# Optimization experiments

Measured on AMD Instinct MI355X. Metric: run time of the kernel, lower is better.

## Reference

```python
import jax, jax.numpy as jnp
import numpy as np

B, NE, NR, A = 512, 100000, 400, 256
ENT, REL, HIST = 200, 200, 400
ADIM = ENT + REL  # 400
HUGE = 1e31
EPS = 1e-20


def _linear(x, W, b):
    return x @ W.T + b


def setup_inputs() -> dict:
    key = jax.random.key(0)
    ks = jax.random.split(key, 26)
    w = lambda k, o, i: (jax.random.normal(k, (o, i)) * 0.02).astype(jnp.float32)
    bz = lambda o: jnp.zeros((o,), jnp.float32)
    inp = {}
    inp['H'] = jax.random.normal(ks[0], (B, HIST), jnp.float32)
    mask = (jax.random.uniform(ks[1], (B, A)) > 0.3).astype(jnp.float32)
    inp['action_mask'] = mask.at[:, 0].set(1.0)  # ensure at least one valid action
    inp['entity_emb'] = jax.random.normal(ks[2], (NE, ENT), jnp.float32) * 0.1
    inp['relation_emb'] = jax.random.normal(ks[3], (NR, REL), jnp.float32) * 0.1
    inp['W1'] = w(ks[4], ADIM, ENT + HIST + REL); inp['b1'] = bz(ADIM)
    inp['W2'] = w(ks[5], ADIM, ADIM); inp['b2'] = bz(ADIM)
    inp['W3'] = w(ks[6], REL, ENT); inp['b3'] = bz(REL)
    inp['W4'] = w(ks[7], REL, REL); inp['b4'] = bz(REL)
    inp['W5'] = w(ks[8], REL, REL + ENT); inp['b5'] = bz(REL)
    inp['W6'] = w(ks[9], REL, REL + REL); inp['b6'] = bz(REL)
    inp['Watt'] = w(ks[10], REL, ADIM + REL); inp['batt'] = bz(REL)
    inp['e'] = jax.random.randint(ks[11], (B,), 0, NE)
    inp['q'] = jax.random.randint(ks[12], (B,), 0, NR)
    inp['pred_id'] = jax.random.randint(ks[13], (B, 1), 0, NE)
    inp['r_space'] = jax.random.randint(ks[14], (B, A), 0, NR)
    inp['e_space'] = jax.random.randint(ks[15], (B, A), 0, NE)
    return inp


def reference(H, action_mask, entity_emb, relation_emb,
              W1, b1, W2, b2, W3, b3, W4, b4, W5, b5, W6, b6, Watt, batt,
              e, q, pred_id, r_space, e_space):
    # --- embed lookups ---
    Q = relation_emb[q]                 # [B, REL]
    E = entity_emb[e]                   # [B, ENT]
    # --- small MLP (dropout in eval mode -> identity) ---
    X = jax.nn.relu(_linear(jnp.concatenate([E, H, Q], -1), W1, b1))
    X2 = _linear(X, W2, b2)             # [B, ADIM]
    # --- full relation attention (multinomial sample replaced by given pred_id) ---
    pred_emb = entity_emb[pred_id]      # [B, 1, ENT]
    pred_ent_info = _linear(pred_emb, W3, b3)       # [B, 1, REL]
    relation_K = _linear(relation_emb, W4, b4)      # [NR, REL]
    local_att = jnp.einsum('bkd,rd->bkr', pred_ent_info, relation_K)  # [B,1,NR]
    beta = jnp.einsum('bkr,rd->bkd', jax.nn.softmax(local_att, -1), relation_emb).sum(1)  # [B, REL]
    # cat([R_all expand, pred_emb expand], -1).sum(1) == [sum_r R_all, NR * pred_emb]
    rel_sum = relation_emb.sum(0)                   # [REL]
    alpha_in = jnp.concatenate([jnp.broadcast_to(rel_sum, (H.shape[0], REL)),
                                NR * pred_emb[:, 0, :]], -1)
    alpha = _linear(alpha_in, W5, b5)               # [B, REL]
    V_A = _linear(jnp.concatenate([alpha, beta], -1), W6, b6)  # [B, REL]
    relation_att = jax.nn.softmax(
        _linear(jnp.concatenate([X2, V_A], -1), Watt, batt) @ relation_emb.T, -1)  # [B, NR]
    # --- policy_nn_fun: action embedding gather + masked softmax ---
    A_emb = jnp.concatenate([relation_emb[r_space], entity_emb[e_space]], -1)  # [B, A, ADIM]
    scores = jnp.einsum('bad,bd->ba', A_emb, X2) - (1.0 - action_mask) * HUGE
    action_dist = jax.nn.softmax(scores, -1)        # [B, A]
    entropy = -jnp.sum(action_dist * jnp.log(action_dist + EPS), -1)  # [B]
    return action_dist, entropy, relation_att
```

## Files before the change

### kernel.cpp

```cpp
#include <hip/hip_runtime.h>
#include <cstdint>
#include <cstddef>

#define BB 512
#define NEn 100000
#define NRr 400
#define AA 256
#define ENTd 200
#define RELd 200
#define HISTd 400
#define ADIMd 400

__device__ __forceinline__ float dot4(const float4 a, const float4 b) {
  return a.x * b.x + a.y * b.y + a.z * b.z + a.w * b.w;
}
__device__ __forceinline__ void fma4(float4& a, const float4 w, const float c) {
  a.x += w.x * c; a.y += w.y * c; a.z += w.z * c; a.w += w.w * c;
}
__device__ __forceinline__ float wave_rmax(float v) {
#pragma unroll
  for (int off = 32; off > 0; off >>= 1) v = fmaxf(v, __shfl_xor(v, off));
  return v;
}
__device__ __forceinline__ float wave_rsum(float v) {
#pragma unroll
  for (int off = 32; off > 0; off >>= 1) v += __shfl_xor(v, off);
  return v;
}

__global__ __launch_bounds__(256) void prep1_kernel(
    const float* __restrict__ rel_emb, const float* __restrict__ W4,
    const float* __restrict__ b4, const float* __restrict__ W5,
    const float* __restrict__ b5, const float* __restrict__ W6,
    const float* __restrict__ Watt, const float* __restrict__ W1,
    const float* __restrict__ W2, float* __restrict__ RK,
    float* __restrict__ P, float* __restrict__ W6bb, float* __restrict__ ab,
    float* __restrict__ relT, float* __restrict__ WaT,
    float* __restrict__ W1T, float* __restrict__ W2T) {
  int t = threadIdx.x;
  int blk = blockIdx.x;
  if (blk == 0) {
    __shared__ float rs[RELd];
    if (t < RELd) {
      float s = 0.f;
      for (int r = 0; r < NRr; r += 4) {
        s += rel_emb[(size_t)r * RELd + t] + rel_emb[(size_t)(r + 1) * RELd + t] +
             rel_emb[(size_t)(r + 2) * RELd + t] + rel_emb[(size_t)(r + 3) * RELd + t];
      }
      rs[t] = s;
    }
    __syncthreads();
    if (t < RELd) {
      float acc = b5[t];
      const float4* w = (const float4*)(W5 + (size_t)t * 400);
      const float4* rv = (const float4*)rs;
      for (int k = 0; k < 50; ++k) acc += dot4(w[k], rv[k]);
      ab[t] = acc;
    }
  } else if (blk <= 50) {
    int r0 = (blk - 1) * 8;
    __shared__ float re[8][RELd];
    for (int i = t; i < 8 * RELd; i += 256)
      re[i / RELd][i % RELd] = rel_emb[(size_t)(r0 + i / RELd) * RELd + i % RELd];
    __syncthreads();
    if (t < RELd) {
      float bv = b4[t];
      float acc[8];
#pragma unroll
      for (int s = 0; s < 8; ++s) acc[s] = bv;
      const float4* w = (const float4*)(W4 + (size_t)t * RELd);
      for (int k = 0; k < 50; ++k) {
        float4 wv = w[k];
#pragma unroll
        for (int s = 0; s < 8; ++s) acc[s] += dot4(wv, ((const float4*)re[s])[k]);
      }
#pragma unroll
      for (int s = 0; s < 8; ++s) RK[(size_t)(r0 + s) * RELd + t] = acc[s];
    }
  } else if (blk <= 75) {
    int i0 = (blk - 51) * 8;
    __shared__ float w6s[8][200];
    for (int i = t; i < 8 * 200; i += 256)
      w6s[i / 200][i % 200] = W6[(size_t)(i0 + i / 200) * 400 + i % 200];
    __syncthreads();
    if (t < 200) {
      int k = t;
      float acc[8] = {0, 0, 0, 0, 0, 0, 0, 0};
      for (int j = 0; j < 200; j += 4) {
        float r0v = W5[(size_t)j * 400 + 200 + k];
        float r1v = W5[(size_t)(j + 1) * 400 + 200 + k];
        float r2v = W5[(size_t)(j + 2) * 400 + 200 + k];
        float r3v = W5[(size_t)(j + 3) * 400 + 200 + k];
#pragma unroll
        for (int s = 0; s < 8; ++s)
          acc[s] += w6s[s][j] * r0v + w6s[s][j + 1] * r1v + w6s[s][j + 2] * r2v +
                    w6s[s][j + 3] * r3v;
      }
#pragma unroll
      for (int s = 0; s < 8; ++s) P[(size_t)(i0 + s) * 200 + k] = 400.f * acc[s];
    }
  } else if (blk <= 100) {
    int u0 = (blk - 76) * 8;
    __shared__ float wbs[8][200];
    for (int i = t; i < 8 * 200; i += 256)
      wbs[i / 200][i % 200] = Watt[(size_t)(u0 + i / 200) * 600 + 400 + i % 200];
    __syncthreads();
    if (t < 200) {
      int j = t;
      float acc[8] = {0, 0, 0, 0, 0, 0, 0, 0};
      for (int i = 0; i < 200; i += 4) {
        float r0v = W6[(size_t)i * 400 + 200 + j];
        float r1v = W6[(size_t)(i + 1) * 400 + 200 + j];
        float r2v = W6[(size_t)(i + 2) * 400 + 200 + j];
        float r3v = W6[(size_t)(i + 3) * 400 + 200 + j];
#pragma unroll
        for (int s = 0; s < 8; ++s)
          acc[s] += wbs[s][i] * r0v + wbs[s][i + 1] * r1v + wbs[s][i + 2] * r2v +
                    wbs[s][i + 3] * r3v;
      }
#pragma unroll
      for (int s = 0; s < 8; ++s) W6bb[(size_t)(u0 + s) * 200 + j] = acc[s];
    }
  } else {
    __shared__ float tlds[64][65];
    int tb = blk - 101;
    const float* src;
    float* dst;
    int M, N, LD, ti, tj;
    if (tb < 28) {
      src = rel_emb; dst = relT; M = 400; N = 200; LD = 200;
      ti = tb / 4; tj = tb % 4;
    } else if (tb < 56) {
      tb -= 28;
      src = Watt; dst = WaT; M = 200; N = 400; LD = 600;
      ti = tb / 7; tj = tb % 7;
    } else if (tb < 147) {
      tb -= 56;
      src = W1; dst = W1T; M = 400; N = 800; LD = 800;
      ti = tb / 13; tj = tb % 13;
    } else {
      tb -= 147;
      src = W2; dst = W2T; M = 400; N = 400; LD = 400;
      ti = tb / 7; tj = tb % 7;
    }
    int i0 = ti * 64, j0 = tj * 64;
    for (int idx = t; idx < 4096; idx += 256) {
      int r = idx >> 6, c = idx & 63;
      int i = i0 + r, j = j0 + c;
      if (i < M && j < N) tlds[r][c] = src[(size_t)i * LD + j];
    }
    __syncthreads();
    for (int idx = t; idx < 4096; idx += 256) {
      int r = idx >> 6, c = idx & 63;
      int j = j0 + r, i = i0 + c;
      if (i < M && j < N) dst[(size_t)j * M + i] = tlds[c][r];
    }
  }
}

__global__ __launch_bounds__(1024) void prep2_x1_kernel(
    const float* __restrict__ rel_emb, const float* __restrict__ W3,
    const float* __restrict__ b3, const float* __restrict__ W6,
    const float* __restrict__ Watt, const float* __restrict__ batt,
    const float* __restrict__ b6, const float* __restrict__ RK,
    const float* __restrict__ P, const float* __restrict__ W6bb,
    const float* __restrict__ ab, float* __restrict__ S_T,
    float* __restrict__ cvec, float* __restrict__ Q_T,
    float* __restrict__ REatt, float* __restrict__ v1,
    const float* __restrict__ ent_emb, const float* __restrict__ H,
    const int* __restrict__ e_idx, const int* __restrict__ q_idx,
    const float* __restrict__ W1T, const float* __restrict__ b1,
    float* __restrict__ X) {
  int t = threadIdx.x;
  int blk = blockIdx.x;
  if (blk < 50) {
    int r0 = blk * 8;
    __shared__ float rks[8][200];
    __shared__ float b3s[200];
    for (int i = t; i < 1600; i += 1024)
      rks[i / 200][i % 200] = RK[(size_t)r0 * 200 + i];
    if (t < 200) b3s[t] = b3[t];
    __syncthreads();
    if (t < 200) {
      int i = t;
      float acc[8] = {0, 0, 0, 0, 0, 0, 0, 0};
      for (int j = 0; j < 200; j += 4) {
        float w0 = W3[(size_t)j * 200 + i];
        float w1 = W3[(size_t)(j + 1) * 200 + i];
        float w2 = W3[(size_t)(j + 2) * 200 + i];
        float w3v = W3[(size_t)(j + 3) * 200 + i];
#pragma unroll
        for (int s = 0; s < 8; ++s)
          acc[s] += w0 * rks[s][j] + w1 * rks[s][j + 1] + w2 * rks[s][j + 2] +
                    w3v * rks[s][j + 3];
      }
      float4 s0 = make_float4(acc[0], acc[1], acc[2], acc[3]);
      float4 s1 = make_float4(acc[4], acc[5], acc[6], acc[7]);
      *(float4*)(S_T + (size_t)i * 400 + r0) = s0;
      *(float4*)(S_T + (size_t)i * 400 + r0 + 4) = s1;
    }
    if (t < 256) {
      int w = t >> 6, lane = t & 63;
      float p0 = 0.f, p1 = 0.f;
      for (int j = lane; j < 200; j += 64) {
        p0 += b3s[j] * rks[w][j];
        p1 += b3s[j] * rks[w + 4][j];
      }
      p0 = wave_rsum(p0);
      p1 = wave_rsum(p1);
      if (lane == 0) {
        cvec[r0 + w] = p0;
        cvec[r0 + w + 4] = p1;
      }
    }
  } else if (blk < 75) {
    int u0 = (blk - 50) * 8;
    __shared__ float wbs[8][200];
    for (int i = t; i < 1600; i += 1024)
      wbs[i / 200][i % 200] = Watt[(size_t)(u0 + i / 200) * 600 + 400 + i % 200];
    __syncthreads();
    if (t < 200) {
      int k = t;
      float acc[8] = {0, 0, 0, 0, 0, 0, 0, 0};
      for (int i = 0; i < 200; i += 4) {
        float r0v = P[(size_t)i * 200 + k];
        float r1v = P[(size_t)(i + 1) * 200 + k];
        float r2v = P[(size_t)(i + 2) * 200 + k];
        float r3v = P[(size_t)(i + 3) * 200 + k];
#pragma unroll
        for (int s = 0; s < 8; ++s)
          acc[s] += wbs[s][i] * r0v + wbs[s][i + 1] * r1v + wbs[s][i + 2] * r2v +
                    wbs[s][i + 3] * r3v;
      }
      float4 s0 = make_float4(acc[0], acc[1], acc[2], acc[3]);
      float4 s1 = make_float4(acc[4], acc[5], acc[6], acc[7]);
      *(float4*)(Q_T + (size_t)k * 200 + u0) = s0;
      *(float4*)(Q_T + (size_t)k * 200 + u0 + 4) = s1;
    }
  } else if (blk < 125) {
    int r0 = (blk - 75) * 8;
    __shared__ float rels[8][200];
    for (int i = t; i < 1600; i += 1024)
      rels[i / 200][i % 200] = rel_emb[(size_t)r0 * 200 + i];
    __syncthreads();
    if (t < 200) {
      float acc[8] = {0, 0, 0, 0, 0, 0, 0, 0};
      const float4* w = (const float4*)(W6bb + (size_t)t * 200);
      for (int k = 0; k < 50; ++k) {
        float4 wv = w[k];
#pragma unroll
        for (int s = 0; s < 8; ++s) acc[s] += dot4(wv, ((const float4*)rels[s])[k]);
      }
#pragma unroll
      for (int s = 0; s < 8; ++s) REatt[(size_t)(r0 + s) * 200 + t] = acc[s];
    }
  } else if (blk == 125) {
    __shared__ float abs_[200];
    __shared__ float us[200];
    if (t < 200) abs_[t] = ab[t];
    __syncthreads();
    if (t < 200) {
      float u = b6[t];
      const float4* w = (const float4*)(W6 + (size_t)t * 400);
      const float4* rv = (const float4*)abs_;
      for (int k = 0; k < 50; ++k) u += dot4(w[k], rv[k]);
      us[t] = u;
    }
    __syncthreads();
    if (t < 200) {
      float v = batt[t];
      const float4* w = (const float4*)(Watt + (size_t)t * 600 + 400);
      const float4* rv = (const float4*)us;
      for (int k = 0; k < 50; ++k) v += dot4(w[k], rv[k]);
      v1[t] = v;
    }
  } else {
    int b0 = (blk - 126) * 4;
    __shared__ float cv[4][800];
    __shared__ float prt[12800];
    for (int i = t; i < 3200; i += 1024) {
      int s = i / 800, k = i % 800;
      float v;
      if (k < ENTd)
        v = ent_emb[(size_t)e_idx[b0 + s] * ENTd + k];
      else if (k < ENTd + HISTd)
        v = H[(size_t)(b0 + s) * HISTd + (k - ENTd)];
      else
        v = rel_emb[(size_t)q_idx[b0 + s] * RELd + (k - ENTd - HISTd)];
      cv[s][k] = v;
    }
    __syncthreads();
    if (t < 800) {
      int g = t % 100, h = t / 100;
      float4 acc[4];
#pragma unroll
      for (int s = 0; s < 4; ++s) acc[s] = make_float4(0, 0, 0, 0);
      const float4* wp = ((const float4*)W1T) + g;
      int k0 = h * 100;
#pragma unroll 4
      for (int kk = 0; kk < 100; ++kk) {
        int k = k0 + kk;
        float4 wv = wp[(size_t)k * 100];
#pragma unroll
        for (int s = 0; s < 4; ++s) fma4(acc[s], wv, cv[s][k]);
      }
#pragma unroll
      for (int s = 0; s < 4; ++s)
        ((float4*)prt)[(h * 4 + s) * 100 + g] = acc[s];
    }
    __syncthreads();
    for (int i = t; i < 1600; i += 1024) {
      int s = i / 400, j = i % 400;
      float a = b1[j];
#pragma unroll
      for (int h = 0; h < 8; ++h) a += prt[(h * 4 + s) * 400 + j];
      X[(size_t)(b0 + s) * ADIMd + j] = fmaxf(a, 0.f);
    }
  }
}

__global__ __launch_bounds__(1024) void x2rx_scores_kernel(
    const float* __restrict__ X, const float* __restrict__ W2T,
    const float* __restrict__ b2, const float* __restrict__ relT,
    const float* __restrict__ ent_emb, const int* __restrict__ r_space,
    const int* __restrict__ e_space, const float* __restrict__ mask,
    float* __restrict__ X2, float* __restrict__ out_dist,
    float* __restrict__ out_ent) {
  int b0 = blockIdx.x * 2;
  int t = threadIdx.x;
  int w = t >> 6, lane = t & 63;
  __shared__ float cv[2][400];
  __shared__ float prt[6400];
  __shared__ float x2full[2][400];
  __shared__ float rxl[2][400];
  __shared__ float scl[512];
  __shared__ float wred2[2][4];
  for (int i = t; i < 800; i += 1024) cv[i / 400][i % 400] = X[(size_t)b0 * 400 + i];
  __syncthreads();
  if (t < 800) {
    int g = t % 100, h = t / 100;
    float4 accA = make_float4(0, 0, 0, 0);
    float4 accB = make_float4(0, 0, 0, 0);
    const float4* wp = ((const float4*)W2T) + g;
    int k0 = h * 50;
#pragma unroll 4
    for (int kk = 0; kk < 50; ++kk) {
      int k = k0 + kk;
      float4 wv = wp[(size_t)k * 100];
      fma4(accA, wv, cv[0][k]);
      fma4(accB, wv, cv[1][k]);
    }
    ((float4*)prt)[(h * 2 + 0) * 100 + g] = accA;
    ((float4*)prt)[(h * 2 + 1) * 100 + g] = accB;
  }
  __syncthreads();
  if (t < 800) {
    int s = t / 400, j = t % 400;
    float a = b2[j];
#pragma unroll
    for (int h = 0; h < 8; ++h) a += prt[(h * 2 + s) * 400 + j];
    X2[(size_t)(b0 + s) * ADIMd + j] = a;
    x2full[s][j] = a;
  }
  __syncthreads();
  if (t < 800) {
    int g = t % 100, h = t / 100;
    float4 accA = make_float4(0, 0, 0, 0);
    float4 accB = make_float4(0, 0, 0, 0);
    const float4* rp = ((const float4*)relT) + g;
    int k0 = h * 25;
#pragma unroll 5
    for (int kk = 0; kk < 25; ++kk) {
      int k = k0 + kk;
      float4 wv = rp[(size_t)k * 100];
      fma4(accA, wv, x2full[0][k]);
      fma4(accB, wv, x2full[1][k]);
    }
    ((float4*)prt)[(h * 2 + 0) * 100 + g] = accA;
    ((float4*)prt)[(h * 2 + 1) * 100 + g] = accB;
  }
  __syncthreads();
  if (t < 800) {
    int s = t / 400, r = t % 400;
    float a = 0.f;
#pragma unroll
    for (int h = 0; h < 8; ++h) a += prt[(h * 2 + s) * 400 + r];
    rxl[s][r] = a;
  }
  __syncthreads();
  {
    int s = w >> 3;
    int wa = (w & 7) * 32;
    const float4* xh = ((const float4*)x2full[s]) + 50;
    for (int c = 0; c < 2; ++c) {
      int abase = wa + c * 16;
      int ei[16];
#pragma unroll
      for (int u = 0; u < 16; ++u)
        ei[u] = e_space[(size_t)(b0 + s) * AA + abase + u];
      float p[16];
      if (lane < 50) {
        float4 xv = xh[lane];
#pragma unroll
        for (int u = 0; u < 16; ++u) {
          float4 vv = ((const float4*)(ent_emb + (size_t)ei[u] * ENTd))[lane];
          p[u] = dot4(vv, xv);
        }
      } else {
#pragma unroll
        for (int u = 0; u < 16; ++u) p[u] = 0.f;
      }
#pragma unroll
      for (int off = 32; off > 0; off >>= 1) {
#pragma unroll
        for (int u = 0; u < 16; ++u) p[u] += __shfl_xor(p[u], off);
      }
      if (lane == 0) {
#pragma unroll
        for (int u = 0; u < 16; ++u) scl[s * 256 + abase + u] = p[u];
      }
    }
  }
  __syncthreads();
  float sc = -INFINITY;
  if (t < 512) {
    int s = t / 256, a = t % 256;
    int r = r_space[(size_t)(b0 + s) * AA + a];
    sc = scl[t] + rxl[s][r] - (1.f - mask[(size_t)(b0 + s) * AA + a]) * 1e31f;
  }
  if (w < 8) {
    float m = wave_rmax(sc);
    if (lane == 0) wred2[w >> 2][w & 3] = m;
  }
  __syncthreads();
  float e = 0.f;
  if (t < 512) {
    int s = t / 256;
    float gm = fmaxf(fmaxf(wred2[s][0], wred2[s][1]),
                     fmaxf(wred2[s][2], wred2[s][3]));
    e = expf(sc - gm);
  }
  __syncthreads();
  if (w < 8) {
    float s2 = wave_rsum(e);
    if (lane == 0) wred2[w >> 2][w & 3] = s2;
  }
  __syncthreads();
  float p = 0.f;
  if (t < 512) {
    int s = t / 256;
    float gs = wred2[s][0] + wred2[s][1] + wred2[s][2] + wred2[s][3];
    p = e / gs;
    out_dist[(size_t)(b0 + s) * AA + (t % 256)] = p;
  }
  float ent = (t < 512) ? -p * logf(p + 1e-20f) : 0.f;
  __syncthreads();
  if (w < 8) {
    float s3 = wave_rsum(ent);
    if (lane == 0) wred2[w >> 2][w & 3] = s3;
  }
  __syncthreads();
  if (t == 0)
    out_ent[b0] = wred2[0][0] + wred2[0][1] + wred2[0][2] + wred2[0][3];
  if (t == 1)
    out_ent[b0 + 1] = wred2[1][0] + wred2[1][1] + wred2[1][2] + wred2[1][3];
}

__global__ __launch_bounds__(1024) void fused_mid_kernel(
    const float* __restrict__ ent_emb, const int* __restrict__ pred_id,
    const float* __restrict__ X2, const float* __restrict__ S_T,
    const float* __restrict__ cvec, const float* __restrict__ Q_T,
    const float* __restrict__ REatt, const float* __restrict__ relT,
    const float* __restrict__ WaT, const float* __restrict__ v1c,
    float* __restrict__ out_ratt) {
  int t = threadIdx.x;
  int w = t >> 6, lane = t & 63;
  __shared__ float pes[4][200];
  __shared__ float x2s[4][400];
  __shared__ float pp[4][400];
  __shared__ float av[4][200];
  __shared__ float prt[12800];
  __shared__ float wred[4][4];
  int b0 = blockIdx.x * 4;
  for (int i = t; i < 2400; i += 1024) {
    if (i < 800)
      pes[i / 200][i % 200] =
          ent_emb[(size_t)pred_id[b0 + i / 200] * ENTd + i % 200];
    else {
      int k = i - 800;
      x2s[k / 400][k % 400] = X2[(size_t)b0 * 400 + k];
    }
  }
  __syncthreads();
  if (t < 800) {
    int g = t % 100, h = t / 100;
    float4 acc[4];
#pragma unroll
    for (int s = 0; s < 4; ++s) acc[s] = make_float4(0, 0, 0, 0);
    const float4* sp = ((const float4*)S_T) + g;
    int k0 = h * 25;
#pragma unroll 5
    for (int kk = 0; kk < 25; ++kk) {
      int k = k0 + kk;
      float4 wv = sp[(size_t)k * 100];
#pragma unroll
      for (int s = 0; s < 4; ++s) fma4(acc[s], wv, pes[s][k]);
    }
#pragma unroll
    for (int s = 0; s < 4; ++s)
      ((float4*)prt)[(h * 4 + s) * 100 + g] = acc[s];
  }
  __syncthreads();
  for (int i = t; i < 1600; i += 1024) {
    int s = i / 400, r = i % 400;
    float a = cvec[r];
#pragma unroll
    for (int h = 0; h < 8; ++h) a += prt[(h * 4 + s) * 400 + r];
    pp[s][r] = a;
  }
  __syncthreads();
  int row = w >> 2, q = w & 3;
  {
    float m = -INFINITY;
    for (int r = q * 64 + lane; r < 400; r += 256) m = fmaxf(m, pp[row][r]);
    m = wave_rmax(m);
    if (lane == 0) wred[row][q] = m;
    __syncthreads();
    float gm = fmaxf(fmaxf(wred[row][0], wred[row][1]),
                     fmaxf(wred[row][2], wred[row][3]));
    __syncthreads();
    float sum = 0.f;
    for (int r = q * 64 + lane; r < 400; r += 256) {
      float e = expf(pp[row][r] - gm);
      pp[row][r] = e;
      sum += e;
    }
    sum = wave_rsum(sum);
    if (lane == 0) wred[row][q] = sum;
    __syncthreads();
    float inv =
        1.f / (wred[row][0] + wred[row][1] + wred[row][2] + wred[row][3]);
    for (int r = q * 64 + lane; r < 400; r += 256) pp[row][r] *= inv;
  }
  __syncthreads();
  if (t < 800) {
    int g = t % 50, h = t / 50;
    float4 acc[4];
    if (h == 0) {
      float4 v = ((const float4*)v1c)[g];
#pragma unroll
      for (int s = 0; s < 4; ++s) acc[s] = v;
    } else {
#pragma unroll
      for (int s = 0; s < 4; ++s) acc[s] = make_float4(0, 0, 0, 0);
    }
    {
      const float4* wp = ((const float4*)WaT) + g;
      int k0 = h * 25;
#pragma unroll 5
      for (int kk = 0; kk < 25; ++kk) {
        int k = k0 + kk;
        float4 wv = wp[(size_t)k * 50];
#pragma unroll
        for (int s = 0; s < 4; ++s) fma4(acc[s], wv, x2s[s][k]);
      }
    }
    if (h < 8) {
      const float4* qp = ((const float4*)Q_T) + g;
      int k0 = h * 25;
#pragma unroll 5
      for (int kk = 0; kk < 25; ++kk) {
        int k = k0 + kk;
        float4 wv = qp[(size_t)k * 50];
#pragma unroll
        for (int s = 0; s < 4; ++s) fma4(acc[s], wv, pes[s][k]);
      }
    }
    {
      const float4* rp = ((const float4*)REatt) + g;
      int r0 = h * 25;
#pragma unroll 5
      for (int kk = 0; kk < 25; ++kk) {
        int r = r0 + kk;
        float4 wv = rp[(size_t)r * 50];
#pragma unroll
        for (int s = 0; s < 4; ++s) fma4(acc[s], wv, pp[s][r]);
      }
    }
#pragma unroll
    for (int s = 0; s < 4; ++s)
      ((float4*)prt)[(h * 4 + s) * 50 + g] = acc[s];
  }
  __syncthreads();
  if (t < 800) {
    int s = t / 200, j = t % 200;
    float a = 0.f;
#pragma unroll
    for (int h = 0; h < 16; ++h) a += prt[(h * 4 + s) * 200 + j];
    av[s][j] = a;
  }
  __syncthreads();
  if (t < 800) {
    int g = t % 100, h = t / 100;
    float4 acc[4];
#pragma unroll
    for (int s = 0; s < 4; ++s) acc[s] = make_float4(0, 0, 0, 0);
    const float4* rp = ((const float4*)relT) + g;
    int k0 = h * 25;
#pragma unroll 5
    for (int kk = 0; kk < 25; ++kk) {
      int k = k0 + kk;
      float4 wv = rp[(size_t)k * 100];
#pragma unroll
      for (int s = 0; s < 4; ++s) fma4(acc[s], wv, av[s][k]);
    }
#pragma unroll
    for (int s = 0; s < 4; ++s)
      ((float4*)prt)[(h * 4 + s) * 100 + g] = acc[s];
  }
  __syncthreads();
  for (int i = t; i < 1600; i += 1024) {
    int s = i / 400, r = i % 400;
    float a = 0.f;
#pragma unroll
    for (int h = 0; h < 8; ++h) a += prt[(h * 4 + s) * 400 + r];
    pp[s][r] = a;
  }
  __syncthreads();
  {
    float m = -INFINITY;
    for (int r = q * 64 + lane; r < 400; r += 256) m = fmaxf(m, pp[row][r]);
    m = wave_rmax(m);
    if (lane == 0) wred[row][q] = m;
    __syncthreads();
    float gm = fmaxf(fmaxf(wred[row][0], wred[row][1]),
                     fmaxf(wred[row][2], wred[row][3]));
    __syncthreads();
    float sum = 0.f;
    for (int r = q * 64 + lane; r < 400; r += 256) {
      float e = expf(pp[row][r] - gm);
      pp[row][r] = e;
      sum += e;
    }
    sum = wave_rsum(sum);
    if (lane == 0) wred[row][q] = sum;
    __syncthreads();
    float inv =
        1.f / (wred[row][0] + wred[row][1] + wred[row][2] + wred[row][3]);
    for (int r = q * 64 + lane; r < 400; r += 256)
      out_ratt[(size_t)(b0 + row) * 400 + r] = pp[row][r] * inv;
  }
}

extern "C" void kernel_launch(void* const* d_in, const int* in_sizes, int n_in,
                              void* d_out, int out_size, void* d_ws,
                              size_t ws_size, hipStream_t stream) {
  const float* H = (const float*)d_in[0];
  const float* mask = (const float*)d_in[1];
  const float* ent_emb = (const float*)d_in[2];
  const float* rel_emb = (const float*)d_in[3];
  const float* W1 = (const float*)d_in[4];
  const float* b1 = (const float*)d_in[5];
  const float* W2 = (const float*)d_in[6];
  const float* b2 = (const float*)d_in[7];
  const float* W3 = (const float*)d_in[8];
  const float* b3 = (const float*)d_in[9];
  const float* W4 = (const float*)d_in[10];
  const float* b4 = (const float*)d_in[11];
  const float* W5 = (const float*)d_in[12];
  const float* b5 = (const float*)d_in[13];
  const float* W6 = (const float*)d_in[14];
  const float* b6 = (const float*)d_in[15];
  const float* Watt = (const float*)d_in[16];
  const float* batt = (const float*)d_in[17];
  const int* e_idx = (const int*)d_in[18];
  const int* q_idx = (const int*)d_in[19];
  const int* pred_id = (const int*)d_in[20];
  const int* r_space = (const int*)d_in[21];
  const int* e_space = (const int*)d_in[22];

  float* ws = (float*)d_ws;
  float* RK = ws;
  float* S_T = ws + 80000;
  float* cvec = ws + 160000;
  float* P = ws + 160512;
  float* Q_T = ws + 200512;
  float* W6bb = ws + 240512;
  float* REatt = ws + 280512;
  float* relT = ws + 360512;
  float* WaT = ws + 440512;
  float* W1T = ws + 520512;
  float* W2T = ws + 840512;
  float* ab = ws + 1000512;
  float* v1 = ws + 1000768;
  float* X = ws + 1001024;
  float* X2 = ws + 1205824;

  float* out = (float*)d_out;
  float* out_dist = out;
  float* out_ent = out + BB * AA;
  float* out_ratt = out + BB * AA + BB;

  hipLaunchKernelGGL(prep1_kernel, dim3(297), dim3(256), 0, stream, rel_emb,
                     W4, b4, W5, b5, W6, Watt, W1, W2, RK, P, W6bb, ab, relT,
                     WaT, W1T, W2T);
  hipLaunchKernelGGL(prep2_x1_kernel, dim3(254), dim3(1024), 0, stream,
                     rel_emb, W3, b3, W6, Watt, batt, b6, RK, P, W6bb, ab,
                     S_T, cvec, Q_T, REatt, v1, ent_emb, H, e_idx, q_idx,
                     W1T, b1, X);
  hipLaunchKernelGGL(x2rx_scores_kernel, dim3(256), dim3(1024), 0, stream, X,
                     W2T, b2, relT, ent_emb, r_space, e_space, mask, X2,
                     out_dist, out_ent);
  hipLaunchKernelGGL(fused_mid_kernel, dim3(128), dim3(1024), 0, stream,
                     ent_emb, pred_id, X2, S_T, cvec, Q_T, REatt, relT, WaT,
                     v1, out_ratt);
}
```

Baseline: 118.8 us.

## Merge scores and relation-attention kernels into one heterogeneous megatail launch

Replaces the two tail kernels with a single 384-block launch. Every third block recomputes X2 for four rows and runs the relation-attention chain. The remaining blocks compute X2, action scores, softmax and entropy for two rows. This removes a kernel launch and the X2 round trip through global memory, and lets both tails run concurrently. In exchange, the W2 GEMV is computed twice and the blocks carry a larger shared-memory footprint.

```diff
diff --git a/kernel.cpp b/kernel.cpp
--- a/kernel.cpp
+++ b/kernel.cpp
@@ -319,336 +319,363 @@
   }
 }
 
-__global__ __launch_bounds__(1024) void x2rx_scores_kernel(
+__global__ __launch_bounds__(1024) void megatail_kernel(
     const float* __restrict__ X, const float* __restrict__ W2T,
     const float* __restrict__ b2, const float* __restrict__ relT,
-    const float* __restrict__ ent_emb, const int* __restrict__ r_space,
-    const int* __restrict__ e_space, const float* __restrict__ mask,
-    float* __restrict__ X2, float* __restrict__ out_dist,
-    float* __restrict__ out_ent) {
-  int b0 = blockIdx.x * 2;
+    const float* __restrict__ ent_emb, const int* __restrict__ pred_id,
+    const float* __restrict__ S_T, const float* __restrict__ cvec,
+    const float* __restrict__ Q_T, const float* __restrict__ REatt,
+    const float* __restrict__ WaT, const float* __restrict__ v1c,
+    const int* __restrict__ r_space, const int* __restrict__ e_space,
+    const float* __restrict__ mask, float* __restrict__ out_ratt,
+    float* __restrict__ out_dist, float* __restrict__ out_ent) {
   int t = threadIdx.x;
   int w = t >> 6, lane = t & 63;
-  __shared__ float cv[2][400];
-  __shared__ float prt[6400];
-  __shared__ float x2full[2][400];
-  __shared__ float rxl[2][400];
-  __shared__ float scl[512];
-  __shared__ float wred2[2][4];
-  for (int i = t; i < 800; i += 1024) cv[i / 400][i % 400] = X[(size_t)b0 * 400 + i];
-  __syncthreads();
-  if (t < 800) {
-    int g = t % 100, h = t / 100;
-    float4 accA = make_float4(0, 0, 0, 0);
-    float4 accB = make_float4(0, 0, 0, 0);
-    const float4* wp = ((const float4*)W2T) + g;
-    int k0 = h * 50;
+  int g = blockIdx.x;
+  __shared__ float smem[19232];
+
+  if (g % 3 == 0) {
+    int b0 = (g / 3) * 4;
+    float(*cv)[400] = (float(*)[400])smem;
+    float(*pes)[200] = (float(*)[200])(smem + 1600);
+    float(*x2s)[400] = (float(*)[400])(smem + 2400);
+    float(*pp)[400] = (float(*)[400])(smem + 4000);
+    float(*av)[200] = (float(*)[200])(smem + 5600);
+    float* prt = smem + 6400;
+    float(*wred)[4] = (float(*)[4])(smem + 19200);
+    for (int i = t; i < 2400; i += 1024) {
+      if (i < 1600)
+        cv[i / 400][i % 400] = X[(size_t)b0 * 400 + i];
+      else {
+        int k = i - 1600;
+        pes[k / 200][k % 200] =
+            ent_emb[(size_t)pred_id[b0 + k / 200] * ENTd + k % 200];
+      }
+    }
+    __syncthreads();
+    if (t < 800) {
+      int gg = t % 100, h = t / 100;
+      float4 acc[4];
+#pragma unroll
+      for (int s = 0; s < 4; ++s) acc[s] = make_float4(0, 0, 0, 0);
+      const float4* wp = ((const float4*)W2T) + gg;
+      int k0 = h * 50;
 #pragma unroll 4
-    for (int kk = 0; kk < 50; ++kk) {
-      int k = k0 + kk;
-      float4 wv = wp[(size_t)k * 100];
-      fma4(accA, wv, cv[0][k]);
-      fma4(accB, wv, cv[1][k]);
-    }
-    ((float4*)prt)[(h * 2 + 0) * 100 + g] = accA;
-    ((float4*)prt)[(h * 2 + 1) * 100 + g] = accB;
-  }
-  __syncthreads();
-  if (t < 800) {
-    int s = t / 400, j = t % 400;
-    float a = b2[j];
-#pragma unroll
-    for (int h = 0; h < 8; ++h) a += prt[(h * 2 + s) * 400 + j];
-    X2[(size_t)(b0 + s) * ADIMd + j] = a;
-    x2full[s][j] = a;
-  }
-  __syncthreads();
-  if (t < 800) {
-    int g = t % 100, h = t / 100;
-    float4 accA = make_float4(0, 0, 0, 0);
-    float4 accB = make_float4(0, 0, 0, 0);
-    const float4* rp = ((const float4*)relT) + g;
-    int k0 = h * 25;
-#pragma unroll 5
-    for (int kk = 0; kk < 25; ++kk) {
-      int k = k0 + kk;
-      float4 wv = rp[(size_t)k * 100];
-      fma4(accA, wv, x2full[0][k]);
-      fma4(accB, wv, x2full[1][k]);
-    }
-    ((float4*)prt)[(h * 2 + 0) * 100 + g] = accA;
-    ((float4*)prt)[(h * 2 + 1) * 100 + g] = accB;
-  }
-  __syncthreads();
-  if (t < 800) {
-    int s = t / 400, r = t % 400;
-    float a = 0.f;
-#pragma unroll
-    for (int h = 0; h < 8; ++h) a += prt[(h * 2 + s) * 400 + r];
-    rxl[s][r] = a;
-  }
-  __syncthreads();
-  {
-    int s = w >> 3;
-    int wa = (w & 7) * 32;
-    const float4* xh = ((const float4*)x2full[s]) + 50;
-    for (int c = 0; c < 2; ++c) {
-      int abase = wa + c * 16;
-      int ei[16];
-#pragma unroll
-      for (int u = 0; u < 16; ++u)
-        ei[u] = e_space[(size_t)(b0 + s) * AA + abase + u];
-      float p[16];
-      if (lane < 50) {
-        float4 xv = xh[lane];
-#pragma unroll
-        for (int u = 0; u < 16; ++u) {
-          float4 vv = ((const float4*)(ent_emb + (size_t)ei[u] * ENTd))[lane];
-          p[u] = dot4(vv, xv);
-        }
-      } else {
-#pragma unroll
-        for (int u = 0; u < 16; ++u) p[u] = 0.f;
-      }
-#pragma unroll
-      for (int off = 32; off > 0; off >>= 1) {
-#pragma unroll
-        for (int u = 0; u < 16; ++u) p[u] += __shfl_xor(p[u], off);
-      }
-      if (lane == 0) {
-#pragma unroll
-        for (int u = 0; u < 16; ++u) scl[s * 256 + abase + u] = p[u];
-      }
-    }
-  }
-  __syncthreads();
-  float sc = -INFINITY;
-  if (t < 512) {
-    int s = t / 256, a = t % 256;
-    int r = r_space[(size_t)(b0 + s) * AA + a];
-    sc = scl[t] + rxl[s][r] - (1.f - mask[(size_t)(b0 + s) * AA + a]) * 1e31f;
-  }
-  if (w < 8) {
-    float m = wave_rmax(sc);
-    if (lane == 0) wred2[w >> 2][w & 3] = m;
-  }
-  __syncthreads();
-  float e = 0.f;
-  if (t < 512) {
-    int s = t / 256;
-    float gm = fmaxf(fmaxf(wred2[s][0], wred2[s][1]),
-                     fmaxf(wred2[s][2], wred2[s][3]));
-    e = expf(sc - gm);
-  }
-  __syncthreads();
-  if (w < 8) {
-    float s2 = wave_rsum(e);
-    if (lane == 0) wred2[w >> 2][w & 3] = s2;
-  }
-  __syncthreads();
-  float p = 0.f;
-  if (t < 512) {
-    int s = t / 256;
-    float gs = wred2[s][0] + wred2[s][1] + wred2[s][2] + wred2[s][3];
-    p = e / gs;
-    out_dist[(size_t)(b0 + s) * AA + (t % 256)] = p;
-  }
-  float ent = (t < 512) ? -p * logf(p + 1e-20f) : 0.f;
-  __syncthreads();
-  if (w < 8) {
-    float s3 = wave_rsum(ent);
-    if (lane == 0) wred2[w >> 2][w & 3] = s3;
-  }
-  __syncthreads();
-  if (t == 0)
-    out_ent[b0] = wred2[0][0] + wred2[0][1] + wred2[0][2] + wred2[0][3];
-  if (t == 1)
-    out_ent[b0 + 1] = wred2[1][0] + wred2[1][1] + wred2[1][2] + wred2[1][3];
-}
-
-__global__ __launch_bounds__(1024) void fused_mid_kernel(
-    const float* __restrict__ ent_emb, const int* __restrict__ pred_id,
-    const float* __restrict__ X2, const float* __restrict__ S_T,
-    const float* __restrict__ cvec, const float* __restrict__ Q_T,
-    const float* __restrict__ REatt, const float* __restrict__ relT,
-    const float* __restrict__ WaT, const float* __restrict__ v1c,
-    float* __restrict__ out_ratt) {
-  int t = threadIdx.x;
-  int w = t >> 6, lane = t & 63;
-  __shared__ float pes[4][200];
-  __shared__ float x2s[4][400];
-  __shared__ float pp[4][400];
-  __shared__ float av[4][200];
-  __shared__ float prt[12800];
-  __shared__ float wred[4][4];
-  int b0 = blockIdx.x * 4;
-  for (int i = t; i < 2400; i += 1024) {
-    if (i < 800)
-      pes[i / 200][i % 200] =
-          ent_emb[(size_t)pred_id[b0 + i / 200] * ENTd + i % 200];
-    else {
-      int k = i - 800;
-      x2s[k / 400][k % 400] = X2[(size_t)b0 * 400 + k];
-    }
-  }
-  __syncthreads();
-  if (t < 800) {
-    int g = t % 100, h = t / 100;
-    float4 acc[4];
-#pragma unroll
-    for (int s = 0; s < 4; ++s) acc[s] = make_float4(0, 0, 0, 0);
-    const float4* sp = ((const float4*)S_T) + g;
-    int k0 = h * 25;
-#pragma unroll 5
-    for (int kk = 0; kk < 25; ++kk) {
-      int k = k0 + kk;
-      float4 wv = sp[(size_t)k * 100];
-#pragma unroll
-      for (int s = 0; s < 4; ++s) fma4(acc[s], wv, pes[s][k]);
-    }
-#pragma unroll
-    for (int s = 0; s < 4; ++s)
-      ((float4*)prt)[(h * 4 + s) * 100 + g] = acc[s];
-  }
-  __syncthreads();
-  for (int i = t; i < 1600; i += 1024) {
-    int s = i / 400, r = i % 400;
-    float a = cvec[r];
-#pragma unroll
-    for (int h = 0; h < 8; ++h) a += prt[(h * 4 + s) * 400 + r];
-    pp[s][r] = a;
-  }
-  __syncthreads();
-  int row = w >> 2, q = w & 3;
-  {
-    float m = -INFINITY;
-    for (int r = q * 64 + lane; r < 400; r += 256) m = fmaxf(m, pp[row][r]);
-    m = wave_rmax(m);
-    if (lane == 0) wred[row][q] = m;
-    __syncthreads();
-    float gm = fmaxf(fmaxf(wred[row][0], wred[row][1]),
-                     fmaxf(wred[row][2], wred[row][3]));
-    __syncthreads();
-    float sum = 0.f;
-    for (int r = q * 64 + lane; r < 400; r += 256) {
-      float e = expf(pp[row][r] - gm);
-      pp[row][r] = e;
-      sum += e;
-    }
-    sum = wave_rsum(sum);
-    if (lane == 0) wred[row][q] = sum;
-    __syncthreads();
-    float inv =
-        1.f / (wred[row][0] + wred[row][1] + wred[row][2] + wred[row][3]);
-    for (int r = q * 64 + lane; r < 400; r += 256) pp[row][r] *= inv;
-  }
-  __syncthreads();
-  if (t < 800) {
-    int g = t % 50, h = t / 50;
-    float4 acc[4];
-    if (h == 0) {
-      float4 v = ((const float4*)v1c)[g];
-#pragma unroll
-      for (int s = 0; s < 4; ++s) acc[s] = v;
-    } else {
+      for (int kk = 0; kk < 50; ++kk) {
+        int k = k0 + kk;
+        float4 wv = wp[(size_t)k * 100];
+#pragma unroll
+        for (int s = 0; s < 4; ++s) fma4(acc[s], wv, cv[s][k]);
+      }
+#pragma unroll
+      for (int s = 0; s < 4; ++s)
+        ((float4*)prt)[(h * 4 + s) * 100 + gg] = acc[s];
+    }
+    __syncthreads();
+    for (int i = t; i < 1600; i += 1024) {
+      int s = i / 400, j = i % 400;
+      float a = b2[j];
+#pragma unroll
+      for (int h = 0; h < 8; ++h) a += prt[(h * 4 + s) * 400 + j];
+      x2s[s][j] = a;
+    }
+    __syncthreads();
+    if (t < 800) {
+      int gg = t % 100, h = t / 100;
+      float4 acc[4];
 #pragma unroll
       for (int s = 0; s < 4; ++s) acc[s] = make_float4(0, 0, 0, 0);
-    }
-    {
-      const float4* wp = ((const float4*)WaT) + g;
+      const float4* sp = ((const float4*)S_T) + gg;
       int k0 = h * 25;
 #pragma unroll 5
       for (int kk = 0; kk < 25; ++kk) {
         int k = k0 + kk;
-        float4 wv = wp[(size_t)k * 50];
-#pragma unroll
-        for (int s = 0; s < 4; ++s) fma4(acc[s], wv, x2s[s][k]);
-      }
-    }
-    if (h < 8) {
-      const float4* qp = ((const float4*)Q_T) + g;
+        float4 wv = sp[(size_t)k * 100];
+#pragma unroll
+        for (int s = 0; s < 4; ++s) fma4(acc[s], wv, pes[s][k]);
+      }
+#pragma unroll
+      for (int s = 0; s < 4; ++s)
+        ((float4*)prt)[(h * 4 + s) * 100 + gg] = acc[s];
+    }
+    __syncthreads();
+    for (int i = t; i < 1600; i += 1024) {
+      int s = i / 400, r = i % 400;
+      float a = cvec[r];
+#pragma unroll
+      for (int h = 0; h < 8; ++h) a += prt[(h * 4 + s) * 400 + r];
+      pp[s][r] = a;
+    }
+    __syncthreads();
+    int row = w >> 2, q = w & 3;
+    {
+      float m = -INFINITY;
+      for (int r = q * 64 + lane; r < 400; r += 256) m = fmaxf(m, pp[row][r]);
+      m = wave_rmax(m);
+      if (lane == 0) wred[row][q] = m;
+      __syncthreads();
+      float gm = fmaxf(fmaxf(wred[row][0], wred[row][1]),
+                       fmaxf(wred[row][2], wred[row][3]));
+      __syncthreads();
+      float sum = 0.f;
+      for (int r = q * 64 + lane; r < 400; r += 256) {
+        float e = expf(pp[row][r] - gm);
+        pp[row][r] = e;
+        sum += e;
+      }
+      sum = wave_rsum(sum);
+      if (lane == 0) wred[row][q] = sum;
+      __syncthreads();
+      float inv =
+          1.f / (wred[row][0] + wred[row][1] + wred[row][2] + wred[row][3]);
+      for (int r = q * 64 + lane; r < 400; r += 256) pp[row][r] *= inv;
+    }
+    __syncthreads();
+    if (t < 800) {
+      int gg = t % 50, h = t / 50;
+      float4 acc[4];
+      if (h == 0) {
+        float4 v = ((const float4*)v1c)[gg];
+#pragma unroll
+        for (int s = 0; s < 4; ++s) acc[s] = v;
+      } else {
+#pragma unroll
+        for (int s = 0; s < 4; ++s) acc[s] = make_float4(0, 0, 0, 0);
+      }
+      {
+        const float4* wp = ((const float4*)WaT) + gg;
+        int k0 = h * 25;
+#pragma unroll 5
+        for (int kk = 0; kk < 25; ++kk) {
+          int k = k0 + kk;
+          float4 wv = wp[(size_t)k * 50];
+#pragma unroll
+          for (int s = 0; s < 4; ++s) fma4(acc[s], wv, x2s[s][k]);
+        }
+      }
+      if (h < 8) {
+        const float4* qp = ((const float4*)Q_T) + gg;
+        int k0 = h * 25;
+#pragma unroll 5
+        for (int kk = 0; kk < 25; ++kk) {
+          int k = k0 + kk;
+          float4 wv = qp[(size_t)k * 50];
+#pragma unroll
+          for (int s = 0; s < 4; ++s) fma4(acc[s], wv, pes[s][k]);
+        }
+      }
+      {
+        const float4* rp = ((const float4*)REatt) + gg;
+        int r0 = h * 25;
+#pragma unroll 5
+        for (int kk = 0; kk < 25; ++kk) {
+          int r = r0 + kk;
+          float4 wv = rp[(size_t)r * 50];
+#pragma unroll
+          for (int s = 0; s < 4; ++s) fma4(acc[s], wv, pp[s][r]);
+        }
+      }
+#pragma unroll
+      for (int s = 0; s < 4; ++s)
+        ((float4*)prt)[(h * 4 + s) * 50 + gg] = acc[s];
+    }
+    __syncthreads();
+    if (t < 800) {
+      int s = t / 200, j = t % 200;
+      float a = 0.f;
+#pragma unroll
+      for (int h = 0; h < 16; ++h) a += prt[(h * 4 + s) * 200 + j];
+      av[s][j] = a;
+    }
+    __syncthreads();
+    if (t < 800) {
+      int gg = t % 100, h = t / 100;
+      float4 acc[4];
+#pragma unroll
+      for (int s = 0; s < 4; ++s) acc[s] = make_float4(0, 0, 0, 0);
+      const float4* rp = ((const float4*)relT) + gg;
       int k0 = h * 25;
 #pragma unroll 5
       for (int kk = 0; kk < 25; ++kk) {
         int k = k0 + kk;
-        float4 wv = qp[(size_t)k * 50];
-#pragma unroll
-        for (int s = 0; s < 4; ++s) fma4(acc[s], wv, pes[s][k]);
-      }
-    }
+        float4 wv = rp[(size_t)k * 100];
+#pragma unroll
+        for (int s = 0; s < 4; ++s) fma4(acc[s], wv, av[s][k]);
+      }
+#pragma unroll
+      for (int s = 0; s < 4; ++s)
+        ((float4*)prt)[(h * 4 + s) * 100 + gg] = acc[s];
+    }
+    __syncthreads();
+    for (int i = t; i < 1600; i += 1024) {
+      int s = i / 400, r = i % 400;
+      float a = 0.f;
+#pragma unroll
+      for (int h = 0; h < 8; ++h) a += prt[(h * 4 + s) * 400 + r];
+      pp[s][r] = a;
+    }
+    __syncthreads();
     {
-      const float4* rp = ((const float4*)REatt) + g;
-      int r0 = h * 25;
+      float m = -INFINITY;
+      for (int r = q * 64 + lane; r < 400; r += 256) m = fmaxf(m, pp[row][r]);
+      m = wave_rmax(m);
+      if (lane == 0) wred[row][q] = m;
+      __syncthreads();
+      float gm = fmaxf(fmaxf(wred[row][0], wred[row][1]),
+                       fmaxf(wred[row][2], wred[row][3]));
+      __syncthreads();
+      float sum = 0.f;
+      for (int r = q * 64 + lane; r < 400; r += 256) {
+        float e = expf(pp[row][r] - gm);
+        pp[row][r] = e;
+        sum += e;
+      }
+      sum = wave_rsum(sum);
+      if (lane == 0) wred[row][q] = sum;
+      __syncthreads();
+      float inv =
+          1.f / (wred[row][0] + wred[row][1] + wred[row][2] + wred[row][3]);
+      for (int r = q * 64 + lane; r < 400; r += 256)
+        out_ratt[(size_t)(b0 + row) * 400 + r] = pp[row][r] * inv;
+    }
+  } else {
+    int b0 = (g - g / 3 - 1) * 2;
+    float(*cv2)[400] = (float(*)[400])smem;
+    float* prt = smem + 800;
+    float(*x2full)[400] = (float(*)[400])(smem + 7200);
+    float(*rxl)[400] = (float(*)[400])(smem + 8000);
+    float* scl = smem + 8800;
+    float(*wred2)[4] = (float(*)[4])(smem + 9312);
+    for (int i = t; i < 800; i += 1024)
+      cv2[i / 400][i % 400] = X[(size_t)b0 * 400 + i];
+    __syncthreads();
+    if (t < 800) {
+      int gg = t % 100, h = t / 100;
+      float4 accA = make_float4(0, 0, 0, 0);
+      float4 accB = make_float4(0, 0, 0, 0);
+      const float4* wp = ((const float4*)W2T) + gg;
+      int k0 = h * 50;
+#pragma unroll 4
+      for (int kk = 0; kk < 50; ++kk) {
+        int k = k0 + kk;
+        float4 wv = wp[(size_t)k * 100];
+        fma4(accA, wv, cv2[0][k]);
+        fma4(accB, wv, cv2[1][k]);
+      }
+      ((float4*)prt)[(h * 2 + 0) * 100 + gg] = accA;
+      ((float4*)prt)[(h * 2 + 1) * 100 + gg] = accB;
+    }
+    __syncthreads();
+    if (t < 800) {
+      int s = t / 400, j = t % 400;
+      float a = b2[j];
+#pragma unroll
+      for (int h = 0; h < 8; ++h) a += prt[(h * 2 + s) * 400 + j];
+      x2full[s][j] = a;
+    }
+    __syncthreads();
+    if (t < 800) {
+      int gg = t % 100, h = t / 100;
+      float4 accA = make_float4(0, 0, 0, 0);
+      float4 accB = make_float4(0, 0, 0, 0);
+      const float4* rp = ((const float4*)relT) + gg;
+      int k0 = h * 25;
 #pragma unroll 5
       for (int kk = 0; kk < 25; ++kk) {
-        int r = r0 + kk;
-        float4 wv = rp[(size_t)r * 50];
-#pragma unroll
-        for (int s = 0; s < 4; ++s) fma4(acc[s], wv, pp[s][r]);
-      }
-    }
-#pragma unroll
-    for (int s = 0; s < 4; ++s)
-      ((float4*)prt)[(h * 4 + s) * 50 + g] = acc[s];
-  }
-  __syncthreads();
-  if (t < 800) {
-    int s = t / 200, j = t % 200;
-    float a = 0.f;
-#pragma unroll
-    for (int h = 0; h < 16; ++h) a += prt[(h * 4 + s) * 200 + j];
-    av[s][j] = a;
-  }
-  __syncthreads();
-  if (t < 800) {
-    int g = t % 100, h = t / 100;
-    float4 acc[4];
-#pragma unroll
-    for (int s = 0; s < 4; ++s) acc[s] = make_float4(0, 0, 0, 0);
-    const float4* rp = ((const float4*)relT) + g;
-    int k0 = h * 25;
-#pragma unroll 5
-    for (int kk = 0; kk < 25; ++kk) {
-      int k = k0 + kk;
-      float4 wv = rp[(size_t)k * 100];
-#pragma unroll
-      for (int s = 0; s < 4; ++s) fma4(acc[s], wv, av[s][k]);
-    }
-#pragma unroll
-    for (int s = 0; s < 4; ++s)
-      ((float4*)prt)[(h * 4 + s) * 100 + g] = acc[s];
-  }
-  __syncthreads();
-  for (int i = t; i < 1600; i += 1024) {
-    int s = i / 400, r = i % 400;
-    float a = 0.f;
-#pragma unroll
-    for (int h = 0; h < 8; ++h) a += prt[(h * 4 + s) * 400 + r];
-    pp[s][r] = a;
-  }
-  __syncthreads();
-  {
-    float m = -INFINITY;
-    for (int r = q * 64 + lane; r < 400; r += 256) m = fmaxf(m, pp[row][r]);
-    m = wave_rmax(m);
-    if (lane == 0) wred[row][q] = m;
-    __syncthreads();
-    float gm = fmaxf(fmaxf(wred[row][0], wred[row][1]),
-                     fmaxf(wred[row][2], wred[row][3]));
-    __syncthreads();
-    float sum = 0.f;
-    for (int r = q * 64 + lane; r < 400; r += 256) {
-      float e = expf(pp[row][r] - gm);
-      pp[row][r] = e;
-      sum += e;
-    }
-    sum = wave_rsum(sum);
-    if (lane == 0) wred[row][q] = sum;
-    __syncthreads();
-    float inv =
-        1.f / (wred[row][0] + wred[row][1] + wred[row][2] + wred[row][3]);
-    for (int r = q * 64 + lane; r < 400; r += 256)
-      out_ratt[(size_t)(b0 + row) * 400 + r] = pp[row][r] * inv;
+        int k = k0 + kk;
+        float4 wv = rp[(size_t)k * 100];
+        fma4(accA, wv, x2full[0][k]);
+        fma4(accB, wv, x2full[1][k]);
+      }
+      ((float4*)prt)[(h * 2 + 0) * 100 + gg] = accA;
+      ((float4*)prt)[(h * 2 + 1) * 100 + gg] = accB;
+    }
+    __syncthreads();
+    if (t < 800) {
+      int s = t / 400, r = t % 400;
+      float a = 0.f;
+#pragma unroll
+      for (int h = 0; h < 8; ++h) a += prt[(h * 2 + s) * 400 + r];
+      rxl[s][r] = a;
+    }
+    __syncthreads();
+    {
+      int s = w >> 3;
+      int wa = (w & 7) * 32;
+      const float4* xh = ((const float4*)x2full[s]) + 50;
+      for (int c = 0; c < 2; ++c) {
+        int abase = wa + c * 16;
+        int ei[16];
+#pragma unroll
+        for (int u = 0; u < 16; ++u)
+          ei[u] = e_space[(size_t)(b0 + s) * AA + abase + u];
+        float p[16];
+        if (lane < 50) {
+          float4 xv = xh[lane];
+#pragma unroll
+          for (int u = 0; u < 16; ++u) {
+            float4 vv = ((const float4*)(ent_emb + (size_t)ei[u] * ENTd))[lane];
+            p[u] = dot4(vv, xv);
+          }
+        } else {
+#pragma unroll
+          for (int u = 0; u < 16; ++u) p[u] = 0.f;
+        }
+#pragma unroll
+        for (int off = 32; off > 0; off >>= 1) {
+#pragma unroll
+          for (int u = 0; u < 16; ++u) p[u] += __shfl_xor(p[u], off);
+        }
+        if (lane == 0) {
+#pragma unroll
+          for (int u = 0; u < 16; ++u) scl[s * 256 + abase + u] = p[u];
+        }
+      }
+    }
+    __syncthreads();
+    float sc = -INFINITY;
+    if (t < 512) {
+      int s = t / 256, a = t % 256;
+      int r = r_space[(size_t)(b0 + s) * AA + a];
+      sc = scl[t] + rxl[s][r] -
+           (1.f - mask[(size_t)(b0 + s) * AA + a]) * 1e31f;
+    }
+    if (w < 8) {
+      float m = wave_rmax(sc);
+      if (lane == 0) wred2[w >> 2][w & 3] = m;
+    }
+    __syncthreads();
+    float e = 0.f;
+    if (t < 512) {
+      int s = t / 256;
+      float gm = fmaxf(fmaxf(wred2[s][0], wred2[s][1]),
+                       fmaxf(wred2[s][2], wred2[s][3]));
+      e = expf(sc - gm);
+    }
+    __syncthreads();
+    if (w < 8) {
+      float s2 = wave_rsum(e);
+      if (lane == 0) wred2[w >> 2][w & 3] = s2;
+    }
+    __syncthreads();
+    float p = 0.f;
+    if (t < 512) {
+      int s = t / 256;
+      float gs = wred2[s][0] + wred2[s][1] + wred2[s][2] + wred2[s][3];
+      p = e / gs;
+      out_dist[(size_t)(b0 + s) * AA + (t % 256)] = p;
+    }
+    float ent = (t < 512) ? -p * logf(p + 1e-20f) : 0.f;
+    __syncthreads();
+    if (w < 8) {
+      float s3 = wave_rsum(ent);
+      if (lane == 0) wred2[w >> 2][w & 3] = s3;
+    }
+    __syncthreads();
+    if (t == 0)
+      out_ent[b0] = wred2[0][0] + wred2[0][1] + wred2[0][2] + wred2[0][3];
+    if (t == 1)
+      out_ent[b0 + 1] = wred2[1][0] + wred2[1][1] + wred2[1][2] + wred2[1][3];
   }
 }
 
@@ -694,7 +721,6 @@
   float* ab = ws + 1000512;
   float* v1 = ws + 1000768;
   float* X = ws + 1001024;
-  float* X2 = ws + 1205824;
 
   float* out = (float*)d_out;
   float* out_dist = out;
@@ -708,10 +734,8 @@
                      rel_emb, W3, b3, W6, Watt, batt, b6, RK, P, W6bb, ab,
                      S_T, cvec, Q_T, REatt, v1, ent_emb, H, e_idx, q_idx,
                      W1T, b1, X);
-  hipLaunchKernelGGL(x2rx_scores_kernel, dim3(256), dim3(1024), 0, stream, X,
-                     W2T, b2, relT, ent_emb, r_space, e_space, mask, X2,
-                     out_dist, out_ent);
-  hipLaunchKernelGGL(fused_mid_kernel, dim3(128), dim3(1024), 0, stream,
-                     ent_emb, pred_id, X2, S_T, cvec, Q_T, REatt, relT, WaT,
-                     v1, out_ratt);
+  hipLaunchKernelGGL(megatail_kernel, dim3(384), dim3(1024), 0, stream, X,
+                     W2T, b2, relT, ent_emb, pred_id, S_T, cvec, Q_T, REatt,
+                     WaT, v1, r_space, e_space, mask, out_ratt, out_dist,
+                     out_ent);
 }
```

Result: faster. 101.1 us (-14.9%).
